# Optimization experiments

Hardware: AMD Instinct MI355X
Metric: run time of the kernel (lower is better)

The kernel has to match this reference:

```python
import jax, jax.numpy as jnp
import numpy as np

IOU_THRESHOLD = 0.3
NUM_CLASSES = 80
BG_IDX = NUM_CLASSES
EPS = 1e-09
TOPK_FALLBACK = 3


def _make_boxes(key, shape, img=640.0):
    # shape = (..., 4); produce valid x1y1x2y2 boxes
    k1, k2 = jax.random.split(key)
    xy = jax.random.uniform(k1, shape[:-1] + (2,)) * img
    wh = jax.random.uniform(k2, shape[:-1] + (2,)) * 128.0 + 8.0
    return jnp.concatenate([xy - wh / 2, xy + wh / 2], axis=-1).astype(jnp.float32)


def setup_inputs() -> dict:
    key = jax.random.key(0)
    ks = jax.random.split(key, 6)
    bs, A, G = 16, 33600, 64
    pd_scores = jax.random.normal(ks[0], (bs, A, NUM_CLASSES), dtype=jnp.float32)
    pd_bboxes = _make_boxes(ks[1], (bs, A, 4))
    anc_points = jax.random.uniform(ks[2], (A, 2), dtype=jnp.float32) * 640.0
    gt_labels = jax.random.randint(ks[3], (bs, G, 1), 0, NUM_CLASSES).astype(jnp.int64)
    gt_bboxes = _make_boxes(ks[4], (bs, G, 4))
    mask_gt = jax.random.randint(ks[5], (bs, G, 1), 0, 2).astype(jnp.int32)
    return {"pd_scores": pd_scores, "pd_bboxes": pd_bboxes, "anc_points": anc_points,
            "gt_labels": gt_labels, "gt_bboxes": gt_bboxes, "mask_gt": mask_gt}


def _pairwise_iou(gt, pd):
    # gt: (bs, G, 4), pd: (bs, A, 4) -> (bs, G, A)
    b1 = gt[:, :, None, :]   # (bs, G, 1, 4)
    b2 = pd[:, None, :, :]   # (bs, 1, A, 4)
    iw = jnp.clip(jnp.minimum(b1[..., 2], b2[..., 2]) - jnp.maximum(b1[..., 0], b2[..., 0]), 0)
    ih = jnp.clip(jnp.minimum(b1[..., 3], b2[..., 3]) - jnp.maximum(b1[..., 1], b2[..., 1]), 0)
    inter = iw * ih
    a1 = (b1[..., 2] - b1[..., 0]) * (b1[..., 3] - b1[..., 1])
    a2 = (b2[..., 2] - b2[..., 0]) * (b2[..., 3] - b2[..., 1])
    return inter / (a1 + a2 - inter + EPS)


def reference(pd_scores, pd_bboxes, anc_points, gt_labels, gt_bboxes, mask_gt):
    bs, G, _ = gt_bboxes.shape
    A = anc_points.shape[0]
    valid = mask_gt[..., 0].astype(bool)                      # (bs, G)

    # IoU matrix; rows of invalid GTs are zero (original writes only valid rows)
    overlaps = _pairwise_iou(gt_bboxes, pd_bboxes) * valid[:, :, None]  # (bs, G, A)

    pos_mask = (overlaps > IOU_THRESHOLD) & valid[:, :, None]
    fg_any = pos_mask.any(axis=(1, 2))                        # (bs,)

    # Per-batch top-k fallback when a batch has zero positives but has valid GTs
    masked = jnp.where(valid[:, :, None], overlaps, -jnp.inf)
    top_vals, _ = jax.lax.top_k(masked.reshape(bs, G * A), TOPK_FALLBACK)
    min_iou = top_vals[:, -1]                                 # (bs,)
    fb_pos = (overlaps >= min_iou[:, None, None]) & valid[:, :, None]
    has_valid = valid.any(axis=1)
    need_fb = (~fg_any) & has_valid
    pos_mask = jnp.where(need_fb[:, None, None], fb_pos, pos_mask)
    fg_mask = pos_mask.any(axis=1)                            # (bs, A)

    # Assignment: argmax over GT axis (first-max, like torch.argmax)
    target_gt_idx = jnp.argmax(overlaps, axis=1)              # (bs, A)

    batch_idx = jnp.arange(bs)[:, None]
    valid_assign = valid[batch_idx, target_gt_idx]            # (bs, A)
    mask = fg_mask & valid_assign

    labels_g = gt_labels[..., 0][batch_idx, target_gt_idx]    # (bs, A)
    target_labels = jnp.where(mask, labels_g, BG_IDX).astype(jnp.int64)
    boxes_g = gt_bboxes[batch_idx, target_gt_idx]             # (bs, A, 4)
    target_bboxes = boxes_g * mask[..., None].astype(boxes_g.dtype)
    # one_hot zeroes out-of-range class indices, matching the explicit range check
    target_scores = jax.nn.one_hot(labels_g, NUM_CLASSES, dtype=jnp.float32) * mask[..., None]

    return (target_labels, target_bboxes, target_scores, fg_mask, target_gt_idx)
```

## Files before the change

kernel.cpp:

```cpp
#include <hip/hip_runtime.h>
#include <math.h>

#define NC 80
constexpr int BS  = 16;
constexpr int NA  = 33600;
constexpr int NG  = 64;
constexpr int TPB = 256;
constexpr int NBLK = (NA + TPB - 1) / TPB;
constexpr int NW   = TPB / 64;
constexpr int NC4  = NC / 4;

typedef float f32x4 __attribute__((ext_vector_type(4)));

__device__ __forceinline__ void ins3(float v, float& t0, float& t1, float& t2) {
  t2 = fmaxf(t2, fminf(v, t1));
  t1 = fmaxf(t1, fminf(v, t0));
  t0 = fmaxf(t0, v);
}

__device__ __forceinline__ void wave_top3(float& t0, float& t1, float& t2) {
  #pragma unroll
  for (int off = 32; off > 0; off >>= 1) {
    float u0 = __shfl_xor(t0, off, 64);
    float u1 = __shfl_xor(t1, off, 64);
    float u2 = __shfl_xor(t2, off, 64);
    ins3(u0, t0, t1, t2);
    ins3(u1, t0, t1, t2);
    ins3(u2, t0, t1, t2);
  }
}

__global__ __launch_bounds__(TPB) void p1_kernel(
    const float4* __restrict__ pd, const float4* __restrict__ gt,
    const int* __restrict__ glab, const int* __restrict__ gmask,
    float* __restrict__ outL, float4* __restrict__ outB,
    float* __restrict__ outS, float* __restrict__ outF,
    float* __restrict__ outI, float* __restrict__ blockTop)
{
  #pragma clang fp contract(off)
  const int b   = blockIdx.y;
  const int tid = threadIdx.x;

  __shared__ float4 sbox[NG];
  __shared__ float  sarea[NG];
  __shared__ int    slab[NG];
  __shared__ int    svalid[NG];

  const int a0  = blockIdx.x * TPB;
  const int a   = a0 + tid;
  const bool inb = a < NA;

  float4 p = make_float4(0.f, 0.f, 0.f, 0.f);
  if (inb) p = pd[(long)b * NA + a];

  if (tid < NG) {
    int v = gmask[b * NG + tid];
    float4 g = gt[b * NG + tid];
    if (!v) g = make_float4(0.f, 0.f, 0.f, 0.f);
    sbox[tid]   = g;
    sarea[tid]  = (g.z - g.x) * (g.w - g.y);
    slab[tid]   = glab[b * NG + tid];
    svalid[tid] = v;
  }
  __syncthreads();

  float best = -1.f;
  int   bidx = 0;
  float a2 = 0.f;
  bool  maskv = false;
  int   blab  = 0;

  if (inb) {
    a2 = (p.z - p.x) * (p.w - p.y);
    #pragma unroll 8
    for (int g = 0; g < NG; ++g) {
      float4 gb = sbox[g];
      float iw = fminf(gb.z, p.z) - fmaxf(gb.x, p.x);
      float ih = fminf(gb.w, p.w) - fmaxf(gb.y, p.y);
      iw = fmaxf(iw, 0.f);
      ih = fmaxf(ih, 0.f);
      float inter = iw * ih;
      float den   = sarea[g] + a2 - inter + 1e-9f;
      float iou   = inter / den;
      bidx = (iou > best) ? g : bidx;
      best = fmaxf(best, iou);
    }
    bool fg = best > 0.3f;
    maskv = fg && (svalid[bidx] != 0);
    blab  = slab[bidx];
    long ga = (long)b * NA + a;
    outL[ga] = maskv ? (float)blab : 80.f;
    float m = maskv ? 1.f : 0.f;
    float4 gb = sbox[bidx];
    outB[ga] = make_float4(gb.x * m, gb.y * m, gb.z * m, gb.w * m);
    outF[ga] = fg ? 1.f : 0.f;
    outI[ga] = (float)bidx;
  }

  const int lane = tid & 63, wid = tid >> 6;
  const int nA    = min(TPB, NA - a0);
  const int wrow0 = wid * 64;
  const int rows  = min(64, nA - wrow0);
  const int own_cls = maskv ? blab : -1;
  if (rows > 0) {
    f32x4* s4 = reinterpret_cast<f32x4*>(outS + ((long)b * NA + a0 + wrow0) * NC);
    const int cnt4 = rows * NC4;
    for (int i = lane; i < cnt4; i += 64) {
      int row = i / NC4;
      int c0  = (i - row * NC4) * 4;
      int cls = __shfl(own_cls, row, 64);
      f32x4 v;
      v.x = (cls == c0    ) ? 1.f : 0.f;
      v.y = (cls == c0 + 1) ? 1.f : 0.f;
      v.z = (cls == c0 + 2) ? 1.f : 0.f;
      v.w = (cls == c0 + 3) ? 1.f : 0.f;
      __builtin_nontemporal_store(v, s4 + i);
    }
  }

  float wmax = best;
  #pragma unroll
  for (int off = 32; off > 0; off >>= 1)
    wmax = fmaxf(wmax, __shfl_xor(wmax, off, 64));

  float* bt = blockTop + (((long)b * NBLK + blockIdx.x) * NW + wid) * 3;

  if (wmax <= 0.3f) {
    float t0 = -INFINITY, t1 = -INFINITY, t2 = -INFINITY;
    if (inb) {
      #pragma unroll 4
      for (int g = 0; g < NG; ++g) {
        float4 gb = sbox[g];
        float iw = fminf(gb.z, p.z) - fmaxf(gb.x, p.x);
        float ih = fminf(gb.w, p.w) - fmaxf(gb.y, p.y);
        iw = fmaxf(iw, 0.f);
        ih = fmaxf(ih, 0.f);
        float inter = iw * ih;
        float den   = sarea[g] + a2 - inter + 1e-9f;
        float iou   = inter / den;
        ins3(iou, t0, t1, t2);
      }
    }
    wave_top3(t0, t1, t2);
    if (lane == 0) { bt[1] = t1; bt[2] = t2; }
  }
  if (lane == 0) bt[0] = wmax;
}

__global__ __launch_bounds__(TPB) void p3_kernel(
    const float4* __restrict__ pd, const float4* __restrict__ gt,
    const int* __restrict__ glab, const int* __restrict__ gmask,
    const float* __restrict__ blockTop,
    float* __restrict__ outL, float4* __restrict__ outB,
    float* __restrict__ outS, float* __restrict__ outF)
{
  #pragma clang fp contract(off)
  const int b   = blockIdx.x;
  const int tid = threadIdx.x;

  __shared__ float  swm[NW];
  __shared__ float  sM;
  __shared__ float  swt[NW][3];
  __shared__ float  sres;
  __shared__ int    sfb;
  __shared__ float4 sbox[NG];
  __shared__ float  sarea[NG];
  __shared__ int    slab[NG];
  __shared__ int    svalid[NG];

  float m = -INFINITY;
  for (int i = tid; i < NBLK * NW; i += TPB)
    m = fmaxf(m, blockTop[((long)b * NBLK * NW + i) * 3]);
  #pragma unroll
  for (int off = 32; off > 0; off >>= 1)
    m = fmaxf(m, __shfl_xor(m, off, 64));
  const int lane = tid & 63, wid = tid >> 6;
  if (lane == 0) swm[wid] = m;
  __syncthreads();
  if (tid == 0) {
    float r = swm[0];
    #pragma unroll
    for (int w = 1; w < NW; ++w) r = fmaxf(r, swm[w]);
    sM = r;
  }
  __syncthreads();
  if (sM > 0.3f) return;

  int gv = (tid < NG) ? gmask[b * NG + tid] : 0;
  unsigned long long bal = __ballot(gv != 0);

  float t0 = -INFINITY, t1 = -INFINITY, t2 = -INFINITY;
  for (int i = tid; i < NBLK * NW; i += TPB) {
    const float* bt = blockTop + ((long)b * NBLK * NW + i) * 3;
    ins3(bt[0], t0, t1, t2);
    ins3(bt[1], t0, t1, t2);
    ins3(bt[2], t0, t1, t2);
  }
  wave_top3(t0, t1, t2);
  if (lane == 0) { swt[wid][0] = t0; swt[wid][1] = t1; swt[wid][2] = t2; }
  __syncthreads();
  if (tid == 0) {
    float r0 = swt[0][0], r1 = swt[0][1], r2 = swt[0][2];
    #pragma unroll
    for (int w = 1; w < NW; ++w) {
      ins3(swt[w][0], r0, r1, r2);
      ins3(swt[w][1], r0, r1, r2);
      ins3(swt[w][2], r0, r1, r2);
    }
    sfb  = (!(r0 > 0.3f) && bal != 0ULL) ? 1 : 0;
    sres = r2;
  }
  if (tid < NG) {
    float4 g = gt[b * NG + tid];
    if (!gv) g = make_float4(0.f, 0.f, 0.f, 0.f);
    sbox[tid]   = g;
    sarea[tid]  = (g.z - g.x) * (g.w - g.y);
    slab[tid]   = glab[b * NG + tid];
    svalid[tid] = gv;
  }
  __syncthreads();
  if (sfb == 0) return;
  const float minio = sres;

  for (int a = tid; a < NA; a += TPB) {
    float4 p  = pd[(long)b * NA + a];
    float  a2 = (p.z - p.x) * (p.w - p.y);
    float best = -1.f;
    int   bidx = 0;
    #pragma unroll 8
    for (int g = 0; g < NG; ++g) {
      float4 gb = sbox[g];
      float iw = fminf(gb.z, p.z) - fmaxf(gb.x, p.x);
      float ih = fminf(gb.w, p.w) - fmaxf(gb.y, p.y);
      iw = fmaxf(iw, 0.f);
      ih = fmaxf(ih, 0.f);
      float inter = iw * ih;
      float den   = sarea[g] + a2 - inter + 1e-9f;
      float iou   = inter / den;
      bidx = (iou > best) ? g : bidx;
      best = fmaxf(best, iou);
    }
    bool fg    = best >= minio;
    bool maskv = fg && (svalid[bidx] != 0);
    int  blab  = slab[bidx];
    long ga = (long)b * NA + a;
    outL[ga] = maskv ? (float)blab : 80.f;
    float mm = maskv ? 1.f : 0.f;
    float4 gb = sbox[bidx];
    outB[ga] = make_float4(gb.x * mm, gb.y * mm, gb.z * mm, gb.w * mm);
    outF[ga] = fg ? 1.f : 0.f;
    if (maskv) outS[ga * NC + blab] = 1.f;
  }
}

extern "C" void kernel_launch(void* const* d_in, const int* in_sizes, int n_in,
                              void* d_out, int out_size, void* d_ws, size_t ws_size,
                              hipStream_t stream) {
  const float4* pd    = (const float4*)d_in[1];
  const int*    glab  = (const int*)d_in[3];
  const float4* gt    = (const float4*)d_in[4];
  const int*    gmask = (const int*)d_in[5];

  float* outf = (float*)d_out;
  float*  outL = outf;
  float4* outB = (float4*)(outf + (long)BS * NA);
  float*  outS = outf + (long)BS * NA * 5;
  float*  outF = outf + (long)BS * NA * 5 + (long)BS * NA * NC;
  float*  outI = outF + (long)BS * NA;

  float* blockTop = (float*)d_ws;

  dim3 grid(NBLK, BS);
  p1_kernel<<<grid, TPB, 0, stream>>>(pd, gt, glab, gmask,
                                      outL, outB, outS, outF, outI, blockTop);
  p3_kernel<<<BS, TPB, 0, stream>>>(pd, gt, glab, gmask, blockTop,
                                    outL, outB, outS, outF);
}
```

Baseline: 282.2 us.

## Fuse fallback pass into main kernel via last-block atomic counter

Replaces the separate per-batch fallback kernel with a last-block-done pattern: each block bumps a per-batch atomic counter after a threadfence, and the final block per batch performs the top-3 reduction and optional fallback reassignment. This removes one kernel launch and its dependency gap, at the cost of an added hipMemsetAsync to reset the counters plus extra shared memory and fences in the main kernel. The fused path is used only if the workspace has room for the counters; otherwise the old two-kernel path remains.

```diff
diff --git a/kernel.cpp b/kernel.cpp
--- a/kernel.cpp
+++ b/kernel.cpp
@@ -35,7 +35,8 @@
     const int* __restrict__ glab, const int* __restrict__ gmask,
     float* __restrict__ outL, float4* __restrict__ outB,
     float* __restrict__ outS, float* __restrict__ outF,
-    float* __restrict__ outI, float* __restrict__ blockTop)
+    float* __restrict__ outI, float* __restrict__ blockTop,
+    int* __restrict__ ctr, int fused)
 {
   #pragma clang fp contract(off)
   const int b   = blockIdx.y;
@@ -45,10 +46,17 @@
   __shared__ float  sarea[NG];
   __shared__ int    slab[NG];
   __shared__ int    svalid[NG];
+  __shared__ int    sLast;
+  __shared__ float  swm[NW];
+  __shared__ float  sM;
+  __shared__ float  swt[NW][3];
+  __shared__ float  sres;
+  __shared__ int    sfb;
 
   const int a0  = blockIdx.x * TPB;
   const int a   = a0 + tid;
   const bool inb = a < NA;
+  const int lane = tid & 63, wid = tid >> 6;
 
   float4 p = make_float4(0.f, 0.f, 0.f, 0.f);
   if (inb) p = pd[(long)b * NA + a];
@@ -97,7 +105,6 @@
     outI[ga] = (float)bidx;
   }
 
-  const int lane = tid & 63, wid = tid >> 6;
   const int nA    = min(TPB, NA - a0);
   const int wrow0 = wid * 64;
   const int rows  = min(64, nA - wrow0);
@@ -145,6 +152,93 @@
     if (lane == 0) { bt[1] = t1; bt[2] = t2; }
   }
   if (lane == 0) bt[0] = wmax;
+
+  if (!fused) return;
+
+  __syncthreads();
+  if (tid == 0) {
+    __threadfence();
+    int old = atomicAdd(&ctr[b], 1);
+    sLast = (old == NBLK - 1) ? 1 : 0;
+  }
+  __syncthreads();
+  if (!sLast) return;
+  __threadfence();
+
+  float m = -INFINITY;
+  for (int i = tid; i < NBLK * NW; i += TPB)
+    m = fmaxf(m, blockTop[((long)b * NBLK * NW + i) * 3]);
+  #pragma unroll
+  for (int off = 32; off > 0; off >>= 1)
+    m = fmaxf(m, __shfl_xor(m, off, 64));
+  if (lane == 0) swm[wid] = m;
+  __syncthreads();
+  if (tid == 0) {
+    float r = swm[0];
+    #pragma unroll
+    for (int w = 1; w < NW; ++w) r = fmaxf(r, swm[w]);
+    sM = r;
+  }
+  __syncthreads();
+  if (sM > 0.3f) return;
+
+  int gv = (tid < NG) ? gmask[b * NG + tid] : 0;
+  unsigned long long bal = __ballot(gv != 0);
+
+  float t0 = -INFINITY, t1 = -INFINITY, t2 = -INFINITY;
+  for (int i = tid; i < NBLK * NW; i += TPB) {
+    const float* btp = blockTop + ((long)b * NBLK * NW + i) * 3;
+    ins3(btp[0], t0, t1, t2);
+    ins3(btp[1], t0, t1, t2);
+    ins3(btp[2], t0, t1, t2);
+  }
+  wave_top3(t0, t1, t2);
+  if (lane == 0) { swt[wid][0] = t0; swt[wid][1] = t1; swt[wid][2] = t2; }
+  __syncthreads();
+  if (tid == 0) {
+    float r0 = swt[0][0], r1 = swt[0][1], r2 = swt[0][2];
+    #pragma unroll
+    for (int w = 1; w < NW; ++w) {
+      ins3(swt[w][0], r0, r1, r2);
+      ins3(swt[w][1], r0, r1, r2);
+      ins3(swt[w][2], r0, r1, r2);
+    }
+    sfb  = (!(r0 > 0.3f) && bal != 0ULL) ? 1 : 0;
+    sres = r2;
+  }
+  __syncthreads();
+  if (sfb == 0) return;
+  const float minio = sres;
+
+  for (int aa = tid; aa < NA; aa += TPB) {
+    float4 pp  = pd[(long)b * NA + aa];
+    float  pa2 = (pp.z - pp.x) * (pp.w - pp.y);
+    float bb = -1.f;
+    int   bi = 0;
+    #pragma unroll 8
+    for (int g = 0; g < NG; ++g) {
+      float4 gb = sbox[g];
+      float iw = fminf(gb.z, pp.z) - fmaxf(gb.x, pp.x);
+      float ih = fminf(gb.w, pp.w) - fmaxf(gb.y, pp.y);
+      iw = fmaxf(iw, 0.f);
+      ih = fmaxf(ih, 0.f);
+      float inter = iw * ih;
+      float den   = sarea[g] + pa2 - inter + 1e-9f;
+      float iou   = inter / den;
+      bi = (iou > bb) ? g : bi;
+      bb = fmaxf(bb, iou);
+    }
+    bool fg    = bb >= minio;
+    bool mk    = fg && (svalid[bi] != 0);
+    int  lb    = slab[bi];
+    long ga = (long)b * NA + aa;
+    outL[ga] = mk ? (float)lb : 80.f;
+    float mm = mk ? 1.f : 0.f;
+    float4 gb = sbox[bi];
+    outB[ga] = make_float4(gb.x * mm, gb.y * mm, gb.z * mm, gb.w * mm);
+    outF[ga] = fg ? 1.f : 0.f;
+    if (mk) outS[ga * NC + lb] = 1.f;
+  }
 }
 
 __global__ __launch_bounds__(TPB) void p3_kernel(
@@ -269,10 +363,18 @@
   float*  outI = outF + (long)BS * NA;
 
   float* blockTop = (float*)d_ws;
+  const size_t btBytes = (size_t)BS * NBLK * NW * 3 * sizeof(float);
+  const size_t ctrOff  = btBytes;
+  const bool   fused   = ws_size >= ctrOff + BS * sizeof(int);
+  int* ctr = (int*)((char*)d_ws + ctrOff);
+
+  if (fused) hipMemsetAsync(ctr, 0, BS * sizeof(int), stream);
 
   dim3 grid(NBLK, BS);
   p1_kernel<<<grid, TPB, 0, stream>>>(pd, gt, glab, gmask,
-                                      outL, outB, outS, outF, outI, blockTop);
-  p3_kernel<<<BS, TPB, 0, stream>>>(pd, gt, glab, gmask, blockTop,
-                                    outL, outB, outS, outF);
-}
+                                      outL, outB, outS, outF, outI,
+                                      blockTop, ctr, fused ? 1 : 0);
+  if (!fused)
+    p3_kernel<<<BS, TPB, 0, stream>>>(pd, gt, glab, gmask, blockTop,
+                                      outL, outB, outS, outF);
+}
```

Result: slower. 371.1 us (+31.5%).
